# Optimization experiments

Measured on AMD Instinct MI355X. Metric: run time of the kernel, lower is better.

## Reference

```python
import jax, jax.numpy as jnp
import numpy as np

H, W = 200, 200            # image_size
X_RANGE = (0.0, 100.0)
Y_RANGE = (0.0, 100.0)
SIZE = 36                   # kernel 'size' from source
SIGMA = 3.0
K = SIZE + 1                # kernel is 37x37 (arange(-18, 19))


def _gaussian_kernel():
    r = jnp.arange(-(SIZE // 2), SIZE // 2 + 1, dtype=jnp.float32)
    k1 = jnp.exp(-(r ** 2) / (2.0 * SIGMA ** 2))
    k2 = k1[:, None] * k1[None, :]
    return k2 / k2.sum()    # [K, K]


def setup_inputs() -> dict:
    key = jax.random.key(0)
    # trajectory coords in world units [0, 100) -> spread over whole map
    x_t = jax.random.uniform(key, (512, 64, 2), dtype=jnp.float32) * 100.0
    return {"x_t": x_t}


def reference(x_t):
    B, T, _ = x_t.shape
    x_scale = W / (X_RANGE[1] - X_RANGE[0])
    y_scale = H / (Y_RANGE[1] - Y_RANGE[0])
    # .long() in torch truncates toward zero; inputs are >= 0 here so astype(int32) matches
    x_pix = ((x_t[:, :, 0] - X_RANGE[0]) * x_scale).astype(jnp.int32)   # [B, T]
    y_pix = H - ((x_t[:, :, 1] - Y_RANGE[0]) * y_scale).astype(jnp.int32)
    valid = ~(jnp.isnan(x_t[:, :, 0]) | jnp.isnan(x_t[:, :, 1]))        # [B, T]

    half = SIZE // 2
    x_start = jnp.clip(x_pix - half, 0, W - SIZE)
    y_start = jnp.clip(y_pix - half, 0, H - SIZE)
    x_end = jnp.clip(x_pix + half, 0, W)
    y_end = jnp.clip(y_pix + half, 0, H)
    kx = x_end - x_start    # patch width  (<= 36, kernel[:,:kx] = top-left slice)
    ky = y_end - y_start    # patch height

    kern = _gaussian_kernel()                       # [K, K]
    r = jnp.arange(K)
    c = jnp.arange(K)
    # mask: kernel[:ky, :kx] slice, and point validity            [B, T, K, K]
    mask = ((r[None, None, :, None] < ky[..., None, None])
            & (c[None, None, None, :] < kx[..., None, None])
            & valid[..., None, None])
    vals = jnp.where(mask, kern[None, None, :, :], 0.0)            # [B, T, K, K]
    rows = jnp.clip(y_start[..., None, None] + r[None, None, :, None], 0, H - 1)
    cols = jnp.clip(x_start[..., None, None] + c[None, None, None, :], 0, W - 1)
    rows = jnp.broadcast_to(rows, (B, T, K, K))
    cols = jnp.broadcast_to(cols, (B, T, K, K))
    flat = (rows * W + cols).reshape(B, -1)                        # [B, T*K*K]

    # parallel scatter-add splat of all Gaussian patches
    heat = jnp.zeros((B, H * W), jnp.float32)
    heat = heat.at[jnp.arange(B)[:, None], flat].add(vals.reshape(B, -1))
    heat = heat.reshape(B, H, W)

    # per-image max normalization (max over dim1 then dim2 == max over both)
    m = heat.max(axis=(1, 2), keepdims=True)
    return heat / (m + 1e-10)
```

## Files before the change

### kernel.cpp

```cpp
#include <hip/hip_runtime.h>


#define NT 64
#define TDIM 224
#define BLK 896

typedef short bf16x8 __attribute__((ext_vector_type(8)));
typedef float f32x4  __attribute__((ext_vector_type(4)));

static __device__ inline unsigned short f2bf(float f) {
    unsigned int u = __float_as_uint(f);
    u = (u + 0x7FFFu + ((u >> 16) & 1u)) >> 16;
    return (unsigned short)u;
}

struct __align__(16) SMem {
    unsigned short Rm[TDIM][64];
    unsigned short Cm[TDIM][64];
    float k1f[37];
    float wmax[14];
};

__global__ __launch_bounds__(BLK, 4) void heatmap_kernel(const float* __restrict__ x_t,
                                                         float* __restrict__ out) {
    __shared__ SMem s;
    const int tid  = threadIdx.x;
    const int lane = tid & 63;
    const int wv   = tid >> 6;
    const int swl  = (lane & 7) << 4;

    if (tid < 37) {
        float sum = 0.0f, mine = 0.0f;
        #pragma unroll
        for (int i = 0; i < 37; ++i) {
            float r = (float)(i - 18);
            float v = expf(-(r * r) * (1.0f / 18.0f));
            sum += v;
            if (i == tid) mine = v;
        }
        s.k1f[tid] = mine / sum;
    }

    for (int img = 0; img < 2; ++img) {
        const int b = 2 * blockIdx.x + img;

        __syncthreads();
        {
            uint4 z = {0u, 0u, 0u, 0u};
            uint4* base = (uint4*)s.Rm;
            #pragma unroll
            for (int i = 0; i < 4; ++i) base[tid + BLK * i] = z;
        }
        __syncthreads();

        {
            const int isC = tid >= 448;
            const int t2  = tid - (isC ? 448 : 0);
            const int p   = t2 / 7;
            const int j   = t2 - 7 * p;
            const float2 xy = *(const float2*)(x_t + (size_t)b * 128 + 2 * p);
            const bool valid = (xy.x == xy.x) && (xy.y == xy.y);
            const int xp = (int)(xy.x * 2.0f);
            const int yp = 200 - (int)(xy.y * 2.0f);
            const int xs = min(max(xp - 18, 0), 164);
            const int ys = min(max(yp - 18, 0), 164);
            const int kx = valid ? (min(max(xp + 18, 0), 200) - xs) : 0;
            const int ky = valid ? (min(max(yp + 18, 0), 200) - ys) : 0;
            const int start = isC ? xs : ys;
            const int len   = isC ? kx : ky;
            char* dst = isC ? (char*)s.Cm : (char*)s.Rm;
            #pragma unroll
            for (int i = 0; i < 6; ++i) {
                const int rel = j * 6 + i;
                if (rel < len) {
                    const int row = start + rel;
                    const int off = (2 * p) ^ ((row & 7) << 4);
                    *(unsigned short*)(dst + row * 128 + off) = f2bf(s.k1f[rel]);
                }
            }
        }
        __syncthreads();

        f32x4 acc[13];
        float gmax = 0.0f;
        if (wv < 13) {
            bf16x8 A0, A1;
            {
                const char* ab = (const char*)s.Rm + (16 * wv + (lane & 15)) * 128;
                A0 = *(const bf16x8*)(ab + ((16 * (lane >> 4)) ^ swl));
                A1 = *(const bf16x8*)(ab + ((16 * (lane >> 4) + 64) ^ swl));
            }
            #pragma unroll
            for (int t = 0; t < 13; ++t) {
                #pragma unroll
                for (int r = 0; r < 4; ++r) acc[t][r] = 0.0f;
            }
            #pragma unroll
            for (int t = 0; t < 13; ++t) {
                const char* bb = (const char*)s.Cm + (16 * t + (lane & 15)) * 128;
                bf16x8 B0 = *(const bf16x8*)(bb + ((16 * (lane >> 4)) ^ swl));
                bf16x8 B1 = *(const bf16x8*)(bb + ((16 * (lane >> 4) + 64) ^ swl));
                acc[t] = __builtin_amdgcn_mfma_f32_16x16x32_bf16(A0, B0, acc[t], 0, 0, 0);
                acc[t] = __builtin_amdgcn_mfma_f32_16x16x32_bf16(A1, B1, acc[t], 0, 0, 0);
            }
            #pragma unroll
            for (int t = 0; t < 13; ++t) {
                #pragma unroll
                for (int r = 0; r < 4; ++r) gmax = fmaxf(gmax, acc[t][r]);
            }
        }
        #pragma unroll
        for (int off = 32; off > 0; off >>= 1) gmax = fmaxf(gmax, __shfl_xor(gmax, off));
        if (lane == 0) s.wmax[wv] = gmax;
        __syncthreads();
        float mm = s.wmax[0];
        #pragma unroll
        for (int w = 1; w < 14; ++w) mm = fmaxf(mm, s.wmax[w]);
        const float scale = 1.0f / (mm + 1e-10f);

        if (wv < 13) {
            float* ob = out + (size_t)b * (200 * 200);
            const int rbase = 16 * wv + 4 * (lane >> 4);
            const int cbase = lane & 15;
            #pragma unroll
            for (int t = 0; t < 13; ++t) {
                const int gcol = 16 * t + cbase;
                #pragma unroll
                for (int r = 0; r < 4; ++r) {
                    const int grow = rbase + r;
                    if (grow < 200 && gcol < 200)
                        ob[(size_t)grow * 200 + gcol] = acc[t][r] * scale;
                }
            }
        }
    }
}

extern "C" void kernel_launch(void* const* d_in, const int* in_sizes, int n_in,
                              void* d_out, int out_size, void* d_ws, size_t ws_size,
                              hipStream_t stream) {
    const float* x_t = (const float*)d_in[0];
    float* out = (float*)d_out;
    const int B = in_sizes[0] / (NT * 2);
    heatmap_kernel<<<B / 2, BLK, 0, stream>>>(x_t, out);
}
```

Measured before the change: 24.56 us.

## Stage output through LDS for coalesced float4 stores, one image per block

```diff
diff --git a/kernel.cpp b/kernel.cpp
--- a/kernel.cpp
+++ b/kernel.cpp
@@ -3,7 +3,7 @@
 
 #define NT 64
 #define TDIM 224
-#define BLK 896
+#define BLK 512
 
 typedef short bf16x8 __attribute__((ext_vector_type(8)));
 typedef float f32x4  __attribute__((ext_vector_type(4)));
@@ -15,10 +15,10 @@
 }
 
 struct __align__(16) SMem {
-    unsigned short Rm[TDIM][64];
-    unsigned short Cm[TDIM][64];
+    unsigned short M[TDIM][64];
+    unsigned short stg[8][16][200];
     float k1f[37];
-    float wmax[14];
+    float wmax[8];
 };
 
 __global__ __launch_bounds__(BLK, 4) void heatmap_kernel(const float* __restrict__ x_t,
@@ -27,8 +27,18 @@
     const int tid  = threadIdx.x;
     const int lane = tid & 63;
     const int wv   = tid >> 6;
+    const int b    = blockIdx.x;
     const int swl  = (lane & 7) << 4;
 
+    {
+        uint4 z = {0u, 0u, 0u, 0u};
+        uint4* base = (uint4*)s.M;
+        #pragma unroll
+        for (int i = 0; i < 4; ++i) {
+            const int idx = tid + BLK * i;
+            if (idx < 1792) base[idx] = z;
+        }
+    }
     if (tid < 37) {
         float sum = 0.0f, mine = 0.0f;
         #pragma unroll
@@ -40,100 +50,134 @@
         }
         s.k1f[tid] = mine / sum;
     }
+    __syncthreads();
 
-    for (int img = 0; img < 2; ++img) {
-        const int b = 2 * blockIdx.x + img;
+    const int p = tid >> 3, j = tid & 7;
+    const float2 xy = *(const float2*)(x_t + (size_t)b * 128 + 2 * p);
+    const bool valid = (xy.x == xy.x) && (xy.y == xy.y);
+    const int xp = (int)(xy.x * 2.0f);
+    const int yp = 200 - (int)(xy.y * 2.0f);
+    const int xs = min(max(xp - 18, 0), 164);
+    const int ys = min(max(yp - 18, 0), 164);
+    const int kx = valid ? (min(max(xp + 18, 0), 200) - xs) : 0;
+    const int ky = valid ? (min(max(yp + 18, 0), 200) - ys) : 0;
 
-        __syncthreads();
-        {
-            uint4 z = {0u, 0u, 0u, 0u};
-            uint4* base = (uint4*)s.Rm;
+    #pragma unroll
+    for (int i = 0; i < 5; ++i) {
+        const int rel = j * 5 + i;
+        if (rel < ky) {
+            const int row = ys + rel;
+            *(unsigned short*)((char*)s.M + row * 128 + ((2 * p) ^ ((row & 7) << 4)))
+                = f2bf(s.k1f[rel]);
+        }
+    }
+    __syncthreads();
+
+    const int s1 = wv, s2 = wv + 8;
+    bf16x8 A10, A11, A20, A21;
+    {
+        const char* ab = (const char*)s.M + (16 * s1 + (lane & 15)) * 128;
+        A10 = *(const bf16x8*)(ab + ((16 * (lane >> 4)) ^ swl));
+        A11 = *(const bf16x8*)(ab + ((16 * (lane >> 4) + 64) ^ swl));
+    }
+    if (s2 < 13) {
+        const char* ab = (const char*)s.M + (16 * s2 + (lane & 15)) * 128;
+        A20 = *(const bf16x8*)(ab + ((16 * (lane >> 4)) ^ swl));
+        A21 = *(const bf16x8*)(ab + ((16 * (lane >> 4) + 64) ^ swl));
+    } else { A20 = A10; A21 = A11; }
+    __syncthreads();
+
+    {
+        uint4 z = {0u, 0u, 0u, 0u};
+        uint4* base = (uint4*)s.M;
+        #pragma unroll
+        for (int i = 0; i < 4; ++i) {
+            const int idx = tid + BLK * i;
+            if (idx < 1792) base[idx] = z;
+        }
+    }
+    __syncthreads();
+    #pragma unroll
+    for (int i = 0; i < 5; ++i) {
+        const int rel = j * 5 + i;
+        if (rel < kx) {
+            const int row = xs + rel;
+            *(unsigned short*)((char*)s.M + row * 128 + ((2 * p) ^ ((row & 7) << 4)))
+                = f2bf(s.k1f[rel]);
+        }
+    }
+    __syncthreads();
+
+    auto compute_strip = [&](bf16x8 A0, bf16x8 A1, f32x4* acc) {
+        #pragma unroll
+        for (int t = 0; t < 13; ++t) {
+            acc[t][0] = 0.0f; acc[t][1] = 0.0f; acc[t][2] = 0.0f; acc[t][3] = 0.0f;
+        }
+        #pragma unroll
+        for (int t = 0; t < 13; ++t) {
+            const char* bb = (const char*)s.M + (16 * t + (lane & 15)) * 128;
+            bf16x8 B0 = *(const bf16x8*)(bb + ((16 * (lane >> 4)) ^ swl));
+            bf16x8 B1 = *(const bf16x8*)(bb + ((16 * (lane >> 4) + 64) ^ swl));
+            acc[t] = __builtin_amdgcn_mfma_f32_16x16x32_bf16(A0, B0, acc[t], 0, 0, 0);
+            acc[t] = __builtin_amdgcn_mfma_f32_16x16x32_bf16(A1, B1, acc[t], 0, 0, 0);
+        }
+    };
+
+    float gmax = 0.0f;
+    {
+        f32x4 acc[13];
+        compute_strip(A10, A11, acc);
+        #pragma unroll
+        for (int t = 0; t < 13; ++t)
             #pragma unroll
-            for (int i = 0; i < 4; ++i) base[tid + BLK * i] = z;
+            for (int r = 0; r < 4; ++r) gmax = fmaxf(gmax, acc[t][r]);
+        if (s2 < 13) {
+            compute_strip(A20, A21, acc);
+            #pragma unroll
+            for (int t = 0; t < 13; ++t)
+                #pragma unroll
+                for (int r = 0; r < 4; ++r) gmax = fmaxf(gmax, acc[t][r]);
         }
-        __syncthreads();
+    }
+    #pragma unroll
+    for (int off = 32; off > 0; off >>= 1) gmax = fmaxf(gmax, __shfl_xor(gmax, off));
+    if (lane == 0) s.wmax[wv] = gmax;
+    __syncthreads();
+    float mm = s.wmax[0];
+    #pragma unroll
+    for (int w = 1; w < 8; ++w) mm = fmaxf(mm, s.wmax[w]);
+    const float scale = 1.0f / (mm + 1e-10f);
 
-        {
-            const int isC = tid >= 448;
-            const int t2  = tid - (isC ? 448 : 0);
-            const int p   = t2 / 7;
-            const int j   = t2 - 7 * p;
-            const float2 xy = *(const float2*)(x_t + (size_t)b * 128 + 2 * p);
-            const bool valid = (xy.x == xy.x) && (xy.y == xy.y);
-            const int xp = (int)(xy.x * 2.0f);
-            const int yp = 200 - (int)(xy.y * 2.0f);
-            const int xs = min(max(xp - 18, 0), 164);
-            const int ys = min(max(yp - 18, 0), 164);
-            const int kx = valid ? (min(max(xp + 18, 0), 200) - xs) : 0;
-            const int ky = valid ? (min(max(yp + 18, 0), 200) - ys) : 0;
-            const int start = isC ? xs : ys;
-            const int len   = isC ? kx : ky;
-            char* dst = isC ? (char*)s.Cm : (char*)s.Rm;
-            #pragma unroll
-            for (int i = 0; i < 6; ++i) {
-                const int rel = j * 6 + i;
-                if (rel < len) {
-                    const int row = start + rel;
-                    const int off = (2 * p) ^ ((row & 7) << 4);
-                    *(unsigned short*)(dst + row * 128 + off) = f2bf(s.k1f[rel]);
-                }
+    float* ob = out + (size_t)b * (200 * 200);
+    unsigned short* st = &s.stg[wv][0][0];
+    auto do_strip = [&](int ss, bf16x8 A0, bf16x8 A1) {
+        f32x4 acc[13];
+        compute_strip(A0, A1, acc);
+        const int r0l = 4 * (lane >> 4), c0l = lane & 15;
+        #pragma unroll
+        for (int t = 0; t < 13; ++t) {
+            const int col = 16 * t + c0l;
+            if (col < 200) {
+                #pragma unroll
+                for (int r = 0; r < 4; ++r)
+                    st[(r0l + r) * 200 + col] = f2bf(acc[t][r] * scale);
             }
         }
-        __syncthreads();
-
-        f32x4 acc[13];
-        float gmax = 0.0f;
-        if (wv < 13) {
-            bf16x8 A0, A1;
-            {
-                const char* ab = (const char*)s.Rm + (16 * wv + (lane & 15)) * 128;
-                A0 = *(const bf16x8*)(ab + ((16 * (lane >> 4)) ^ swl));
-                A1 = *(const bf16x8*)(ab + ((16 * (lane >> 4) + 64) ^ swl));
-            }
-            #pragma unroll
-            for (int t = 0; t < 13; ++t) {
-                #pragma unroll
-                for (int r = 0; r < 4; ++r) acc[t][r] = 0.0f;
-            }
-            #pragma unroll
-            for (int t = 0; t < 13; ++t) {
-                const char* bb = (const char*)s.Cm + (16 * t + (lane & 15)) * 128;
-                bf16x8 B0 = *(const bf16x8*)(bb + ((16 * (lane >> 4)) ^ swl));
-                bf16x8 B1 = *(const bf16x8*)(bb + ((16 * (lane >> 4) + 64) ^ swl));
-                acc[t] = __builtin_amdgcn_mfma_f32_16x16x32_bf16(A0, B0, acc[t], 0, 0, 0);
-                acc[t] = __builtin_amdgcn_mfma_f32_16x16x32_bf16(A1, B1, acc[t], 0, 0, 0);
-            }
-            #pragma unroll
-            for (int t = 0; t < 13; ++t) {
-                #pragma unroll
-                for (int r = 0; r < 4; ++r) gmax = fmaxf(gmax, acc[t][r]);
-            }
+        __threadfence_block();
+        const int nrow = min(16, 200 - 16 * ss);
+        float* obs = ob + (size_t)(16 * ss) * 200;
+        for (int i = lane; i < nrow * 50; i += 64) {
+            uint2 v = *(const uint2*)(st + 4 * i);
+            float4 o;
+            o.x = __uint_as_float(v.x << 16);
+            o.y = __uint_as_float(v.x & 0xFFFF0000u);
+            o.z = __uint_as_float(v.y << 16);
+            o.w = __uint_as_float(v.y & 0xFFFF0000u);
+            *(float4*)(obs + 4 * i) = o;
         }
-        #pragma unroll
-        for (int off = 32; off > 0; off >>= 1) gmax = fmaxf(gmax, __shfl_xor(gmax, off));
-        if (lane == 0) s.wmax[wv] = gmax;
-        __syncthreads();
-        float mm = s.wmax[0];
-        #pragma unroll
-        for (int w = 1; w < 14; ++w) mm = fmaxf(mm, s.wmax[w]);
-        const float scale = 1.0f / (mm + 1e-10f);
-
-        if (wv < 13) {
-            float* ob = out + (size_t)b * (200 * 200);
-            const int rbase = 16 * wv + 4 * (lane >> 4);
-            const int cbase = lane & 15;
-            #pragma unroll
-            for (int t = 0; t < 13; ++t) {
-                const int gcol = 16 * t + cbase;
-                #pragma unroll
-                for (int r = 0; r < 4; ++r) {
-                    const int grow = rbase + r;
-                    if (grow < 200 && gcol < 200)
-                        ob[(size_t)grow * 200 + gcol] = acc[t][r] * scale;
-                }
-            }
-        }
-    }
+    };
+    do_strip(s1, A10, A11);
+    if (s2 < 13) do_strip(s2, A20, A21);
 }
 
 extern "C" void kernel_launch(void* const* d_in, const int* in_sizes, int n_in,
@@ -142,5 +186,5 @@
     const float* x_t = (const float*)d_in[0];
     float* out = (float*)d_out;
     const int B = in_sizes[0] / (NT * 2);
-    heatmap_kernel<<<B / 2, BLK, 0, stream>>>(x_t, out);
+    heatmap_kernel<<<B, BLK, 0, stream>>>(x_t, out);
 }
```

After: 23.33 us. 1.05x faster.
